# Optimization experiments

Measured on AMD Instinct MI355X. Metric: run time of the kernel, lower is better.

## Reference

```python
import jax, jax.numpy as jnp
import numpy as np

E, B, DX, DC, DH, DO = 16, 4096, 128, 64, 1024, 128
DIN = DX + DC

def setup_inputs() -> dict:
    key = jax.random.key(0)
    ks = jax.random.split(key, 6)
    s1 = 1.0 / np.sqrt(DIN)
    s2 = 1.0 / np.sqrt(DH)
    return {
        "x": jax.random.normal(ks[0], (E, B, DX), dtype=jnp.float32),
        "cond": jax.random.normal(ks[1], (E, B, DC), dtype=jnp.float32),
        # stacked per-expert params, mirroring param_stacks ([E, ...])
        "W1": jax.random.uniform(ks[2], (E, DH, DIN), minval=-s1, maxval=s1, dtype=jnp.float32),
        "b1": jax.random.uniform(ks[3], (E, DH), minval=-s1, maxval=s1, dtype=jnp.float32),
        "W2": jax.random.uniform(ks[4], (E, DO, DH), minval=-s2, maxval=s2, dtype=jnp.float32),
        "b2": jax.random.uniform(ks[5], (E, DO), minval=-s2, maxval=s2, dtype=jnp.float32),
    }

def reference(x, cond, W1, b1, W2, b2):
    # vmap over experts == grouped GEMM with per-expert weight tiles
    xc = jnp.concatenate([x, cond], axis=-1)          # [E, B, DIN]
    h = jnp.einsum('ebi,ehi->ebh', xc, W1) + b1[:, None, :]  # [E, B, DH]
    h = jax.nn.relu(h)
    y = jnp.einsum('ebh,eoh->ebo', h, W2) + b2[:, None, :]   # [E, B, DO]
    return y
```

## Files before the change

### kernel.cpp

```cpp
#include <hip/hip_runtime.h>
#include <hip/hip_bf16.h>

#define E_   16
#define B_   4096
#define DX_  128
#define DC_  64
#define DIN_ 192
#define DH_  1024
#define DO_  128

#define BM 256
#define KC 64
#define NCHUNK (DH_ / KC)
#define NT 1024

#define W1B_OFF 0
#define W1B_STR 12288
#define W2B_OFF 24576
#define W2B_STR 8192
#define HB_OFF  40960
#define HB_STR  16384

#define NW1U2 (E_ * DH_ * DIN_ / 4)
#define NW2U2 (E_ * DO_ * DH_ / 4)
#define WS_BYTES ((size_t)(NW1U2 + NW2U2) * 8)

typedef __attribute__((ext_vector_type(4))) float f32x4;
typedef __attribute__((ext_vector_type(8))) short bf16x8;

__device__ __forceinline__ unsigned f2bf_u(float f) {
    union { float f; unsigned u; } v; v.f = f;
    return (v.u + 0x7fffu + ((v.u >> 16) & 1u)) >> 16;
}
__device__ __forceinline__ uint2 pack4(float4 v) {
    uint2 r;
    r.x = f2bf_u(v.x) | (f2bf_u(v.y) << 16);
    r.y = f2bf_u(v.z) | (f2bf_u(v.w) << 16);
    return r;
}
__device__ __forceinline__ int swz(int r, int S, int cb) {
    return r * S + ((cb ^ ((r & 7) << 4)) >> 1);
}

__global__ __launch_bounds__(256)
void convert_w(const float4* __restrict__ W1, const float4* __restrict__ W2,
               uint2* __restrict__ ws) {
    const int ntot = NW1U2 + NW2U2;
    for (int i = blockIdx.x * 256 + threadIdx.x; i < ntot; i += gridDim.x * 256) {
        float4 v = (i < NW1U2) ? W1[i] : W2[i - NW1U2];
        ws[i] = pack4(v);
    }
}

template <bool WS>
__global__ __launch_bounds__(NT, 4)
void moe_fused_kernel(const float* __restrict__ x, const float* __restrict__ cond,
                      const float* __restrict__ W1, const float* __restrict__ b1,
                      const float* __restrict__ W2, const float* __restrict__ b2,
                      const uint2* __restrict__ wsw, float* __restrict__ out) {
    __shared__ short LDSU[73728];

    const int bid = blockIdx.x;
    const int xcd = bid & 7;
    const int s   = bid >> 3;
    const int e   = 2 * xcd + (s & 1);
    const int row0 = (s >> 1) * BM;

    const int tid  = threadIdx.x;
    const int w    = tid >> 6;
    const int lane = tid & 63;
    const int lr   = lane & 15;
    const int lg   = lane >> 4;
    const int wr   = w >> 2, wc2 = w & 3;

    const uint2*  ws1 = wsw + (size_t)e * (DH_ * DIN_ / 4);
    const uint2*  ws2 = wsw + NW1U2 + (size_t)e * (DO_ * DH_ / 4);
    const float4* g1f = (const float4*)(W1 + (size_t)e * DH_ * DIN_);
    const float*  g2f = W2 + (size_t)e * DO_ * DH_;

    uint2 r1[3]; float4 r1f[3];
    uint2 r2[2]; float4 r2f[2];

    if constexpr (WS) {
#pragma unroll
        for (int i = 0; i < 3; ++i) r1[i] = ws1[tid + NT * i];
    } else {
#pragma unroll
        for (int i = 0; i < 3; ++i) r1f[i] = g1f[tid + NT * i];
    }

    {
        const float4* gx = (const float4*)(x + (size_t)(e * B_ + row0) * DX_);
#pragma unroll
        for (int i = 0; i < 8; ++i) {
            int g = tid + NT * i;
            int r = g >> 5, c = g & 31;
            *(uint2*)&LDSU[swz(r, DIN_, c * 8)] = pack4(gx[g]);
        }
        const float4* gc = (const float4*)(cond + (size_t)(e * B_ + row0) * DC_);
#pragma unroll
        for (int i = 0; i < 4; ++i) {
            int g = tid + NT * i;
            int r = g >> 4, c = g & 15;
            *(uint2*)&LDSU[128 + swz(r, DIN_, c * 8)] = pack4(gc[g]);
        }
    }
    __syncthreads();

    bf16x8 xcreg[6];
#pragma unroll
    for (int kk = 0; kk < 6; ++kk)
        xcreg[kk] = *(const bf16x8*)&LDSU[swz(w * 16 + lr, DIN_, kk * 64 + lg * 16)];
    __syncthreads();

#pragma unroll
    for (int i = 0; i < 3; ++i) {
        int g = tid + NT * i;
        int r = g / 48, cc = g - r * 48;
        uint2 pv; if constexpr (WS) pv = r1[i]; else pv = pack4(r1f[i]);
        *(uint2*)&LDSU[W1B_OFF + swz(r, DIN_, cc * 8)] = pv;
    }
    if constexpr (WS) {
#pragma unroll
        for (int i = 0; i < 3; ++i) r1[i] = ws1[3072 + tid + NT * i];
#pragma unroll
        for (int i = 0; i < 2; ++i) {
            int g = tid + NT * i;
            int r = g >> 4, cc = g & 15;
            r2[i] = ws2[r * 256 + cc];
        }
    } else {
#pragma unroll
        for (int i = 0; i < 3; ++i) r1f[i] = g1f[3072 + tid + NT * i];
#pragma unroll
        for (int i = 0; i < 2; ++i) {
            int g = tid + NT * i;
            int r = g >> 4, cc = g & 15;
            r2f[i] = *(const float4*)(g2f + (size_t)r * DH_ + cc * 4);
        }
    }
    __syncthreads();

    f32x4 acc2[4][2] = {};

    for (int c = 0; c < NCHUNK; ++c) {
        const int pc = c & 1, pp = pc ^ 1;

        float b1v[4];
#pragma unroll
        for (int nf = 0; nf < 4; ++nf)
            b1v[nf] = b1[e * DH_ + c * KC + nf * 16 + lr];

#pragma unroll
        for (int i = 0; i < 2; ++i) {
            int g = tid + NT * i;
            int r = g >> 4, cc = g & 15;
            uint2 pv; if constexpr (WS) pv = r2[i]; else pv = pack4(r2f[i]);
            *(uint2*)&LDSU[W2B_OFF + pc * W2B_STR + swz(r, KC, cc * 8)] = pv;
        }
        if (c + 1 < NCHUNK) {
#pragma unroll
            for (int i = 0; i < 3; ++i) {
                int g = tid + NT * i;
                int r = g / 48, cc = g - r * 48;
                uint2 pv; if constexpr (WS) pv = r1[i]; else pv = pack4(r1f[i]);
                *(uint2*)&LDSU[W1B_OFF + pp * W1B_STR + swz(r, DIN_, cc * 8)] = pv;
            }
        }
        if (c + 2 < NCHUNK) {
            if constexpr (WS) {
#pragma unroll
                for (int i = 0; i < 3; ++i) r1[i] = ws1[(c + 2) * 3072 + tid + NT * i];
            } else {
#pragma unroll
                for (int i = 0; i < 3; ++i) r1f[i] = g1f[(c + 2) * 3072 + tid + NT * i];
            }
        }
        if (c + 1 < NCHUNK) {
            if constexpr (WS) {
#pragma unroll
                for (int i = 0; i < 2; ++i) {
                    int g = tid + NT * i;
                    int r = g >> 4, cc = g & 15;
                    r2[i] = ws2[r * 256 + (c + 1) * 16 + cc];
                }
            } else {
#pragma unroll
                for (int i = 0; i < 2; ++i) {
                    int g = tid + NT * i;
                    int r = g >> 4, cc = g & 15;
                    r2f[i] = *(const float4*)(g2f + (size_t)r * DH_ + (c + 1) * KC + cc * 4);
                }
            }
        }

        if (c > 0) {
#pragma unroll
            for (int kk = 0; kk < KC / 32; ++kk) {
                bf16x8 af[4], bfr[2];
#pragma unroll
                for (int mf = 0; mf < 4; ++mf)
                    af[mf] = *(const bf16x8*)&LDSU[HB_OFF + pp * HB_STR + swz(wr * 64 + mf * 16 + lr, KC, kk * 64 + lg * 16)];
#pragma unroll
                for (int nf = 0; nf < 2; ++nf)
                    bfr[nf] = *(const bf16x8*)&LDSU[W2B_OFF + pp * W2B_STR + swz(wc2 * 32 + nf * 16 + lr, KC, kk * 64 + lg * 16)];
#pragma unroll
                for (int mf = 0; mf < 4; ++mf)
#pragma unroll
                    for (int nf = 0; nf < 2; ++nf)
                        acc2[mf][nf] = __builtin_amdgcn_mfma_f32_16x16x32_bf16(af[mf], bfr[nf], acc2[mf][nf], 0, 0, 0);
            }
        }

        f32x4 acc1[4] = {};
#pragma unroll
        for (int kk = 0; kk < DIN_ / 32; ++kk) {
            bf16x8 bfr[4];
#pragma unroll
            for (int nf = 0; nf < 4; ++nf)
                bfr[nf] = *(const bf16x8*)&LDSU[W1B_OFF + pc * W1B_STR + swz(nf * 16 + lr, DIN_, kk * 64 + lg * 16)];
#pragma unroll
            for (int nf = 0; nf < 4; ++nf)
                acc1[nf] = __builtin_amdgcn_mfma_f32_16x16x32_bf16(xcreg[kk], bfr[nf], acc1[nf], 0, 0, 0);
        }
#pragma unroll
        for (int nf = 0; nf < 4; ++nf)
#pragma unroll
            for (int j = 0; j < 4; ++j) {
                float v = fmaxf(acc1[nf][j] + b1v[nf], 0.f);
                int hr = w * 16 + lg * 4 + j;
                int hc = nf * 16 + lr;
                LDSU[HB_OFF + pc * HB_STR + swz(hr, KC, 2 * hc)] = (short)f2bf_u(v);
            }

        __syncthreads();
    }

    {
        const int pl = (NCHUNK - 1) & 1;
#pragma unroll
        for (int kk = 0; kk < KC / 32; ++kk) {
            bf16x8 af[4], bfr[2];
#pragma unroll
            for (int mf = 0; mf < 4; ++mf)
                af[mf] = *(const bf16x8*)&LDSU[HB_OFF + pl * HB_STR + swz(wr * 64 + mf * 16 + lr, KC, kk * 64 + lg * 16)];
#pragma unroll
            for (int nf = 0; nf < 2; ++nf)
                bfr[nf] = *(const bf16x8*)&LDSU[W2B_OFF + pl * W2B_STR + swz(wc2 * 32 + nf * 16 + lr, KC, kk * 64 + lg * 16)];
#pragma unroll
            for (int mf = 0; mf < 4; ++mf)
#pragma unroll
                for (int nf = 0; nf < 2; ++nf)
                    acc2[mf][nf] = __builtin_amdgcn_mfma_f32_16x16x32_bf16(af[mf], bfr[nf], acc2[mf][nf], 0, 0, 0);
        }
    }

    float b2v[2];
#pragma unroll
    for (int nf = 0; nf < 2; ++nf)
        b2v[nf] = b2[e * DO_ + wc2 * 32 + nf * 16 + lr];
#pragma unroll
    for (int mf = 0; mf < 4; ++mf)
#pragma unroll
        for (int nf = 0; nf < 2; ++nf)
#pragma unroll
            for (int j = 0; j < 4; ++j) {
                int m = wr * 64 + mf * 16 + lg * 4 + j;
                int o = wc2 * 32 + nf * 16 + lr;
                out[(size_t)(e * B_ + row0 + m) * DO_ + o] = acc2[mf][nf][j] + b2v[nf];
            }
}

extern "C" void kernel_launch(void* const* d_in, const int* in_sizes, int n_in,
                              void* d_out, int out_size, void* d_ws, size_t ws_size,
                              hipStream_t stream) {
    const float* x    = (const float*)d_in[0];
    const float* cond = (const float*)d_in[1];
    const float* W1   = (const float*)d_in[2];
    const float* b1   = (const float*)d_in[3];
    const float* W2   = (const float*)d_in[4];
    const float* b2   = (const float*)d_in[5];
    float* out = (float*)d_out;

    dim3 grid(E_ * (B_ / BM));
    dim3 block(NT);

    const bool usews = (ws_size >= WS_BYTES) && (d_ws != nullptr);
    if (usews) {
        convert_w<<<2560, 256, 0, stream>>>((const float4*)W1, (const float4*)W2,
                                            (uint2*)d_ws);
        moe_fused_kernel<true><<<grid, block, 0, stream>>>(
            x, cond, W1, b1, W2, b2, (const uint2*)d_ws, out);
    } else {
        moe_fused_kernel<false><<<grid, block, 0, stream>>>(
            x, cond, W1, b1, W2, b2, (const uint2*)nullptr, out);
    }
}
```

Before: 170.9 us.

## Pre-swizzle W1 chunks and stream them via direct global-to-LDS loads; transpose MFMA operands

The weight conversion pass now writes W1 in the per-chunk swizzled LDS layout, so the fused kernel can copy each chunk straight into LDS with global_load_lds and no longer stages it through registers. x and cond are loaded and converted directly into registers, which removes the LDS staging pass and its two barriers. Both GEMMs swap their MFMA operand roles (weights as A, activations as B), so the hidden tile is written packed (4 values per store) and the output as float4 with vectorised bias loads. The main risk is that the async LDS loads are not explicitly waited on before the barrier, which could race if the compiler does not insert a vmcnt wait.

```diff
diff --git a/kernel.cpp b/kernel.cpp
--- a/kernel.cpp
+++ b/kernel.cpp
@@ -11,7 +11,7 @@
 
 #define BM 256
 #define KC 64
-#define NCHUNK (DH_ / KC)
+#define NCHUNK 16
 #define NT 1024
 
 #define W1B_OFF 0
@@ -41,14 +41,38 @@
 __device__ __forceinline__ int swz(int r, int S, int cb) {
     return r * S + ((cb ^ ((r & 7) << 4)) >> 1);
 }
+__device__ __forceinline__ bf16x8 load8cvt(const float* p) {
+    float4 a = *(const float4*)p;
+    float4 b = *(const float4*)(p + 4);
+    bf16x8 r;
+    r[0] = (short)f2bf_u(a.x); r[1] = (short)f2bf_u(a.y);
+    r[2] = (short)f2bf_u(a.z); r[3] = (short)f2bf_u(a.w);
+    r[4] = (short)f2bf_u(b.x); r[5] = (short)f2bf_u(b.y);
+    r[6] = (short)f2bf_u(b.z); r[7] = (short)f2bf_u(b.w);
+    return r;
+}
+__device__ __forceinline__ void gld_lds16(const void* g, void* l) {
+    __builtin_amdgcn_global_load_lds(
+        (const __attribute__((address_space(1))) unsigned int*)g,
+        (__attribute__((address_space(3))) unsigned int*)l, 16, 0, 0);
+}
 
 __global__ __launch_bounds__(256)
 void convert_w(const float4* __restrict__ W1, const float4* __restrict__ W2,
                uint2* __restrict__ ws) {
     const int ntot = NW1U2 + NW2U2;
     for (int i = blockIdx.x * 256 + threadIdx.x; i < ntot; i += gridDim.x * 256) {
-        float4 v = (i < NW1U2) ? W1[i] : W2[i - NW1U2];
-        ws[i] = pack4(v);
+        if (i < NW1U2) {
+            float4 v = W1[i];
+            int e  = i / (DH_ * 48);
+            int rr = i - e * (DH_ * 48);
+            int hr = rr / 48, cu = rr - hr * 48;
+            int ch = hr >> 6, r = hr & 63;
+            int S  = swz(r, DIN_, cu * 8);
+            ws[(size_t)(e * 16 + ch) * 3072 + (S >> 2)] = pack4(v);
+        } else {
+            ws[i] = pack4(W2[i - NW1U2]);
+        }
     }
 }
 
@@ -71,71 +95,47 @@
     const int lane = tid & 63;
     const int lr   = lane & 15;
     const int lg   = lane >> 4;
-    const int wr   = w >> 2, wc2 = w & 3;
-
-    const uint2*  ws1 = wsw + (size_t)e * (DH_ * DIN_ / 4);
-    const uint2*  ws2 = wsw + NW1U2 + (size_t)e * (DO_ * DH_ / 4);
+    const int wo   = w & 1;
+    const int wm   = w >> 1;
+
+    const char*  ws1b = (const char*)wsw;
+    const uint2* ws2  = wsw + NW1U2 + (size_t)e * (DO_ * DH_ / 4);
     const float4* g1f = (const float4*)(W1 + (size_t)e * DH_ * DIN_);
     const float*  g2f = W2 + (size_t)e * DO_ * DH_;
 
-    uint2 r1[3]; float4 r1f[3];
-    uint2 r2[2]; float4 r2f[2];
-
+    bf16x8 xcreg[6];
+    {
+        const float* xrow = x    + (size_t)(e * B_ + row0 + w * 16 + lr) * DX_;
+        const float* crow = cond + (size_t)(e * B_ + row0 + w * 16 + lr) * DC_;
+#pragma unroll
+        for (int kk = 0; kk < 4; ++kk) xcreg[kk] = load8cvt(xrow + kk * 32 + lg * 8);
+#pragma unroll
+        for (int kk = 4; kk < 6; ++kk) xcreg[kk] = load8cvt(crow + (kk - 4) * 32 + lg * 8);
+    }
+
+    uint2  r2[2]; float4 r2f[2]; float4 r1f[3];
     if constexpr (WS) {
-#pragma unroll
-        for (int i = 0; i < 3; ++i) r1[i] = ws1[tid + NT * i];
+        for (int q = w; q < 24; q += 16)
+            gld_lds16(ws1b + (size_t)(e * 16 + 0) * 24576 + q * 1024 + lane * 16,
+                      (char*)&LDSU[W1B_OFF] + q * 1024);
+#pragma unroll
+        for (int i = 0; i < 2; ++i) {
+            int g = tid + NT * i, r = g >> 4, cc = g & 15;
+            r2[i] = ws2[r * 256 + cc];
+        }
     } else {
 #pragma unroll
         for (int i = 0; i < 3; ++i) r1f[i] = g1f[tid + NT * i];
-    }
-
-    {
-        const float4* gx = (const float4*)(x + (size_t)(e * B_ + row0) * DX_);
-#pragma unroll
-        for (int i = 0; i < 8; ++i) {
-            int g = tid + NT * i;
-            int r = g >> 5, c = g & 31;
-            *(uint2*)&LDSU[swz(r, DIN_, c * 8)] = pack4(gx[g]);
-        }
-        const float4* gc = (const float4*)(cond + (size_t)(e * B_ + row0) * DC_);
-#pragma unroll
-        for (int i = 0; i < 4; ++i) {
-            int g = tid + NT * i;
-            int r = g >> 4, c = g & 15;
-            *(uint2*)&LDSU[128 + swz(r, DIN_, c * 8)] = pack4(gc[g]);
-        }
-    }
-    __syncthreads();
-
-    bf16x8 xcreg[6];
-#pragma unroll
-    for (int kk = 0; kk < 6; ++kk)
-        xcreg[kk] = *(const bf16x8*)&LDSU[swz(w * 16 + lr, DIN_, kk * 64 + lg * 16)];
-    __syncthreads();
-
-#pragma unroll
-    for (int i = 0; i < 3; ++i) {
-        int g = tid + NT * i;
-        int r = g / 48, cc = g - r * 48;
-        uint2 pv; if constexpr (WS) pv = r1[i]; else pv = pack4(r1f[i]);
-        *(uint2*)&LDSU[W1B_OFF + swz(r, DIN_, cc * 8)] = pv;
-    }
-    if constexpr (WS) {
-#pragma unroll
-        for (int i = 0; i < 3; ++i) r1[i] = ws1[3072 + tid + NT * i];
+#pragma unroll
+        for (int i = 0; i < 3; ++i) {
+            int g = tid + NT * i, r = g / 48, cu = g - r * 48;
+            *(uint2*)&LDSU[W1B_OFF + swz(r, DIN_, cu * 8)] = pack4(r1f[i]);
+        }
+#pragma unroll
+        for (int i = 0; i < 3; ++i) r1f[i] = g1f[3072 + tid + NT * i];
 #pragma unroll
         for (int i = 0; i < 2; ++i) {
-            int g = tid + NT * i;
-            int r = g >> 4, cc = g & 15;
-            r2[i] = ws2[r * 256 + cc];
-        }
-    } else {
-#pragma unroll
-        for (int i = 0; i < 3; ++i) r1f[i] = g1f[3072 + tid + NT * i];
-#pragma unroll
-        for (int i = 0; i < 2; ++i) {
-            int g = tid + NT * i;
-            int r = g >> 4, cc = g & 15;
+            int g = tid + NT * i, r = g >> 4, cc = g & 15;
             r2f[i] = *(const float4*)(g2f + (size_t)r * DH_ + cc * 4);
         }
     }
@@ -146,49 +146,40 @@
     for (int c = 0; c < NCHUNK; ++c) {
         const int pc = c & 1, pp = pc ^ 1;
 
-        float b1v[4];
-#pragma unroll
-        for (int nf = 0; nf < 4; ++nf)
-            b1v[nf] = b1[e * DH_ + c * KC + nf * 16 + lr];
-
 #pragma unroll
         for (int i = 0; i < 2; ++i) {
-            int g = tid + NT * i;
-            int r = g >> 4, cc = g & 15;
+            int g = tid + NT * i, r = g >> 4, cc = g & 15;
             uint2 pv; if constexpr (WS) pv = r2[i]; else pv = pack4(r2f[i]);
             *(uint2*)&LDSU[W2B_OFF + pc * W2B_STR + swz(r, KC, cc * 8)] = pv;
         }
         if (c + 1 < NCHUNK) {
-#pragma unroll
-            for (int i = 0; i < 3; ++i) {
-                int g = tid + NT * i;
-                int r = g / 48, cc = g - r * 48;
-                uint2 pv; if constexpr (WS) pv = r1[i]; else pv = pack4(r1f[i]);
-                *(uint2*)&LDSU[W1B_OFF + pp * W1B_STR + swz(r, DIN_, cc * 8)] = pv;
-            }
-        }
-        if (c + 2 < NCHUNK) {
             if constexpr (WS) {
-#pragma unroll
-                for (int i = 0; i < 3; ++i) r1[i] = ws1[(c + 2) * 3072 + tid + NT * i];
+                for (int q = w; q < 24; q += 16)
+                    gld_lds16(ws1b + (size_t)(e * 16 + c + 1) * 24576 + q * 1024 + lane * 16,
+                              (char*)&LDSU[W1B_OFF + pp * W1B_STR] + q * 1024);
             } else {
 #pragma unroll
-                for (int i = 0; i < 3; ++i) r1f[i] = g1f[(c + 2) * 3072 + tid + NT * i];
+                for (int i = 0; i < 3; ++i) {
+                    int g = tid + NT * i, r = g / 48, cu = g - r * 48;
+                    *(uint2*)&LDSU[W1B_OFF + pp * W1B_STR + swz(r, DIN_, cu * 8)] = pack4(r1f[i]);
+                }
+                if (c + 2 < NCHUNK) {
+#pragma unroll
+                    for (int i = 0; i < 3; ++i) r1f[i] = g1f[(c + 2) * 3072 + tid + NT * i];
+                }
             }
         }
         if (c + 1 < NCHUNK) {
             if constexpr (WS) {
 #pragma unroll
                 for (int i = 0; i < 2; ++i) {
-                    int g = tid + NT * i;
-                    int r = g >> 4, cc = g & 15;
+                    int g = tid + NT * i, r = g >> 4, cc = g & 15;
                     r2[i] = ws2[r * 256 + (c + 1) * 16 + cc];
                 }
             } else {
 #pragma unroll
                 for (int i = 0; i < 2; ++i) {
-                    int g = tid + NT * i;
-                    int r = g >> 4, cc = g & 15;
+                    int g = tid + NT * i, r = g >> 4, cc = g & 15;
                     r2f[i] = *(const float4*)(g2f + (size_t)r * DH_ + (c + 1) * KC + cc * 4);
                 }
             }
@@ -196,79 +187,80 @@
 
         if (c > 0) {
 #pragma unroll
-            for (int kk = 0; kk < KC / 32; ++kk) {
-                bf16x8 af[4], bfr[2];
-#pragma unroll
-                for (int mf = 0; mf < 4; ++mf)
-                    af[mf] = *(const bf16x8*)&LDSU[HB_OFF + pp * HB_STR + swz(wr * 64 + mf * 16 + lr, KC, kk * 64 + lg * 16)];
+            for (int kk = 0; kk < 2; ++kk) {
+                bf16x8 aW2[4], bH[2];
+#pragma unroll
+                for (int of = 0; of < 4; ++of)
+                    aW2[of] = *(const bf16x8*)&LDSU[W2B_OFF + pp * W2B_STR + swz(wo * 64 + of * 16 + lr, KC, kk * 64 + lg * 16)];
 #pragma unroll
                 for (int nf = 0; nf < 2; ++nf)
-                    bfr[nf] = *(const bf16x8*)&LDSU[W2B_OFF + pp * W2B_STR + swz(wc2 * 32 + nf * 16 + lr, KC, kk * 64 + lg * 16)];
-#pragma unroll
-                for (int mf = 0; mf < 4; ++mf)
+                    bH[nf] = *(const bf16x8*)&LDSU[HB_OFF + pp * HB_STR + swz(wm * 32 + nf * 16 + lr, KC, kk * 64 + lg * 16)];
+#pragma unroll
+                for (int of = 0; of < 4; ++of)
 #pragma unroll
                     for (int nf = 0; nf < 2; ++nf)
-                        acc2[mf][nf] = __builtin_amdgcn_mfma_f32_16x16x32_bf16(af[mf], bfr[nf], acc2[mf][nf], 0, 0, 0);
+                        acc2[of][nf] = __builtin_amdgcn_mfma_f32_16x16x32_bf16(aW2[of], bH[nf], acc2[of][nf], 0, 0, 0);
             }
         }
 
         f32x4 acc1[4] = {};
 #pragma unroll
-        for (int kk = 0; kk < DIN_ / 32; ++kk) {
-            bf16x8 bfr[4];
-#pragma unroll
-            for (int nf = 0; nf < 4; ++nf)
-                bfr[nf] = *(const bf16x8*)&LDSU[W1B_OFF + pc * W1B_STR + swz(nf * 16 + lr, DIN_, kk * 64 + lg * 16)];
-#pragma unroll
-            for (int nf = 0; nf < 4; ++nf)
-                acc1[nf] = __builtin_amdgcn_mfma_f32_16x16x32_bf16(xcreg[kk], bfr[nf], acc1[nf], 0, 0, 0);
-        }
-#pragma unroll
-        for (int nf = 0; nf < 4; ++nf)
-#pragma unroll
-            for (int j = 0; j < 4; ++j) {
-                float v = fmaxf(acc1[nf][j] + b1v[nf], 0.f);
-                int hr = w * 16 + lg * 4 + j;
-                int hc = nf * 16 + lr;
-                LDSU[HB_OFF + pc * HB_STR + swz(hr, KC, 2 * hc)] = (short)f2bf_u(v);
-            }
+        for (int kk = 0; kk < 6; ++kk) {
+            bf16x8 aW[4];
+#pragma unroll
+            for (int hf = 0; hf < 4; ++hf)
+                aW[hf] = *(const bf16x8*)&LDSU[W1B_OFF + pc * W1B_STR + swz(hf * 16 + lr, DIN_, kk * 64 + lg * 16)];
+#pragma unroll
+            for (int hf = 0; hf < 4; ++hf)
+                acc1[hf] = __builtin_amdgcn_mfma_f32_16x16x32_bf16(aW[hf], xcreg[kk], acc1[hf], 0, 0, 0);
+        }
+#pragma unroll
+        for (int hf = 0; hf < 4; ++hf) {
+            float4 b1f = *(const float4*)&b1[e * DH_ + c * KC + hf * 16 + lg * 4];
+            float v0 = fmaxf(acc1[hf][0] + b1f.x, 0.f);
+            float v1 = fmaxf(acc1[hf][1] + b1f.y, 0.f);
+            float v2 = fmaxf(acc1[hf][2] + b1f.z, 0.f);
+            float v3 = fmaxf(acc1[hf][3] + b1f.w, 0.f);
+            uint2 hv;
+            hv.x = f2bf_u(v0) | (f2bf_u(v1) << 16);
+            hv.y = f2bf_u(v2) | (f2bf_u(v3) << 16);
+            int m = w * 16 + lr;
+            *(uint2*)&LDSU[HB_OFF + pc * HB_STR + swz(m, KC, hf * 32 + lg * 8)] = hv;
+        }
 
         __syncthreads();
     }
 
-    {
-        const int pl = (NCHUNK - 1) & 1;
-#pragma unroll
-        for (int kk = 0; kk < KC / 32; ++kk) {
-            bf16x8 af[4], bfr[2];
-#pragma unroll
-            for (int mf = 0; mf < 4; ++mf)
-                af[mf] = *(const bf16x8*)&LDSU[HB_OFF + pl * HB_STR + swz(wr * 64 + mf * 16 + lr, KC, kk * 64 + lg * 16)];
+#pragma unroll
+    for (int kk = 0; kk < 2; ++kk) {
+        bf16x8 aW2[4], bH[2];
+#pragma unroll
+        for (int of = 0; of < 4; ++of)
+            aW2[of] = *(const bf16x8*)&LDSU[W2B_OFF + W2B_STR + swz(wo * 64 + of * 16 + lr, KC, kk * 64 + lg * 16)];
+#pragma unroll
+        for (int nf = 0; nf < 2; ++nf)
+            bH[nf] = *(const bf16x8*)&LDSU[HB_OFF + HB_STR + swz(wm * 32 + nf * 16 + lr, KC, kk * 64 + lg * 16)];
+#pragma unroll
+        for (int of = 0; of < 4; ++of)
 #pragma unroll
             for (int nf = 0; nf < 2; ++nf)
-                bfr[nf] = *(const bf16x8*)&LDSU[W2B_OFF + pl * W2B_STR + swz(wc2 * 32 + nf * 16 + lr, KC, kk * 64 + lg * 16)];
-#pragma unroll
-            for (int mf = 0; mf < 4; ++mf)
-#pragma unroll
-                for (int nf = 0; nf < 2; ++nf)
-                    acc2[mf][nf] = __builtin_amdgcn_mfma_f32_16x16x32_bf16(af[mf], bfr[nf], acc2[mf][nf], 0, 0, 0);
-        }
-    }
-
-    float b2v[2];
-#pragma unroll
-    for (int nf = 0; nf < 2; ++nf)
-        b2v[nf] = b2[e * DO_ + wc2 * 32 + nf * 16 + lr];
-#pragma unroll
-    for (int mf = 0; mf < 4; ++mf)
-#pragma unroll
-        for (int nf = 0; nf < 2; ++nf)
-#pragma unroll
-            for (int j = 0; j < 4; ++j) {
-                int m = wr * 64 + mf * 16 + lg * 4 + j;
-                int o = wc2 * 32 + nf * 16 + lr;
-                out[(size_t)(e * B_ + row0 + m) * DO_ + o] = acc2[mf][nf][j] + b2v[nf];
-            }
+                acc2[of][nf] = __builtin_amdgcn_mfma_f32_16x16x32_bf16(aW2[of], bH[nf], acc2[of][nf], 0, 0, 0);
+    }
+
+#pragma unroll
+    for (int of = 0; of < 4; ++of) {
+        float4 b2f = *(const float4*)&b2[e * DO_ + wo * 64 + of * 16 + lg * 4];
+#pragma unroll
+        for (int nf = 0; nf < 2; ++nf) {
+            int m = wm * 32 + nf * 16 + lr;
+            float4 val;
+            val.x = acc2[of][nf][0] + b2f.x;
+            val.y = acc2[of][nf][1] + b2f.y;
+            val.z = acc2[of][nf][2] + b2f.z;
+            val.w = acc2[of][nf][3] + b2f.w;
+            *(float4*)&out[(size_t)(e * B_ + row0 + m) * DO_ + wo * 64 + of * 16 + lg * 4] = val;
+        }
+    }
 }
 
 extern "C" void kernel_launch(void* const* d_in, const int* in_sizes, int n_in,
```

New measurement: 155.3 us. 9.1% less time.
